# Kernel tuning notes

Measured on AMD Instinct MI355X. Metric: run time of the kernel, lower is better.

The kernel has to match this reference:

```python
import jax, jax.numpy as jnp
import numpy as np

M, K, N = 8192, 4096, 4096
ALPHA, BETA = 0.002, 0.0005


def setup_inputs() -> dict:
    key = jax.random.key(0)
    kx, kw, kb = jax.random.split(key, 3)
    # int8-range quantized activations and weights (stored as int32 for portability)
    x = jax.random.randint(kx, (M, K), -127, 127, dtype=jnp.int32)
    weight = jax.random.randint(kw, (N, K), -127, 127, dtype=jnp.int32)  # (out, in)
    bias = jax.random.randint(kb, (1, N), -(2**20), 2**20, dtype=jnp.int32)
    alpha = jnp.float32(ALPHA)
    beta = jnp.float32(BETA)
    return {"x": x, "weight": weight, "bias": bias, "alpha": alpha, "beta": beta}


def reference(x, weight, bias, alpha, beta):
    # int8 GEMM with int32 accumulation: acc[m, n] = sum_k x[m, k] * W[n, k]
    acc = jnp.matmul(x, weight.T, preferred_element_type=jnp.int32)  # [M, N] int32
    # CUTLASS-style epilogue: D = round(alpha * acc + beta * bias) -> int32
    y = alpha * acc.astype(jnp.float32) + beta * bias.astype(jnp.float32)
    return jnp.round(y).astype(jnp.int32)
```

## Files before the change

### kernel.cpp

```cpp
#include <hip/hip_runtime.h>
#include <hip/hip_bf16.h>
#include <stdint.h>

#define M_DIM 8192
#define N_DIM 4096
#define K_DIM 4096

#define BM 256
#define BN 256
#define BK 64
#define NT (K_DIM / BK)
#define DEPTH 4

typedef int v4i __attribute__((ext_vector_type(4)));

#define AS1C(p) ((const __attribute__((address_space(1))) void*)(p))
#define AS3(p)  ((__attribute__((address_space(3))) void*)(p))

__device__ __forceinline__ int pack4(int a, int b, int c, int d) {
  return (a & 0xff) | ((b & 0xff) << 8) | ((c & 0xff) << 16) | (d << 24);
}

__global__ void pack_both_kernel(const int* __restrict__ x, const int* __restrict__ w,
                                 char* __restrict__ A8, char* __restrict__ B8,
                                 int nA, int nTot) {
  int idx = blockIdx.x * blockDim.x + threadIdx.x;
  int stride = gridDim.x * blockDim.x;
  for (int i = idx; i < nTot; i += stride) {
    const int4* pin;
    int4* pout;
    if (i < nA) {
      pin  = (const int4*)x + 4 * (size_t)i;
      pout = (int4*)A8 + i;
    } else {
      int j = i - nA;
      pin  = (const int4*)w + 4 * (size_t)j;
      pout = (int4*)B8 + j;
    }
    int4 v0 = pin[0];
    int4 v1 = pin[1];
    int4 v2 = pin[2];
    int4 v3 = pin[3];
    int4 o;
    o.x = pack4(v0.x, v0.y, v0.z, v0.w);
    o.y = pack4(v1.x, v1.y, v1.z, v1.w);
    o.z = pack4(v2.x, v2.y, v2.z, v2.w);
    o.w = pack4(v3.x, v3.y, v3.z, v3.w);
    *pout = o;
  }
}

__global__ __launch_bounds__(512, 2) void gemm_i8_kernel(
    const char* __restrict__ A8, const char* __restrict__ B8,
    const int* __restrict__ bias, const float* __restrict__ alpha_p,
    const float* __restrict__ beta_p, int* __restrict__ out) {
  __shared__ alignas(16) char lds[DEPTH][BM * BK + BN * BK];

  const int tid  = threadIdx.x;
  const int lane = tid & 63;
  const int wave = tid >> 6;

  const int orig = blockIdx.x;
  const int swz  = (orig & 7) * (512 / 8) + (orig >> 3);
  const int bm   = (swz >> 4) * BM;
  const int bn   = (swz & 15) * BN;

  int aoff[2], boff[2], ldsoff[2];
#pragma unroll
  for (int i = 0; i < 2; ++i) {
    int linear = i * 8192 + tid * 16;
    int row = linear >> 6;
    int p   = (linear >> 4) & 3;
    int g   = p ^ ((row >> 1) & 3);
    ldsoff[i] = i * 8192 + wave * 1024;
    aoff[i] = (bm + row) * K_DIM + g * 16;
    boff[i] = (bn + row) * K_DIM + g * 16;
  }

#define STAGE_A(t)                                                                  \
  do {                                                                              \
    const char* ab_ = A8 + (t) * BK;                                                \
    char* base_ = &lds[(t) & (DEPTH - 1)][0];                                       \
    _Pragma("unroll") for (int i_ = 0; i_ < 2; ++i_)                                \
      __builtin_amdgcn_global_load_lds(AS1C(ab_ + aoff[i_]),                        \
                                       AS3(base_ + ldsoff[i_]), 16, 0, 0);          \
  } while (0)

#define STAGE_B(t)                                                                  \
  do {                                                                              \
    const char* bb_ = B8 + (t) * BK;                                                \
    char* base_ = &lds[(t) & (DEPTH - 1)][0];                                       \
    _Pragma("unroll") for (int i_ = 0; i_ < 2; ++i_)                                \
      __builtin_amdgcn_global_load_lds(AS1C(bb_ + boff[i_]),                        \
                                       AS3(base_ + 16384 + ldsoff[i_]), 16, 0, 0);  \
  } while (0)

  v4i acc[8][4];
#pragma unroll
  for (int i = 0; i < 8; ++i)
#pragma unroll
    for (int j = 0; j < 4; ++j) acc[i][j] = (v4i){0, 0, 0, 0};

  const int wr = wave >> 2;
  const int wc = wave & 3;
  const int frow = lane & 15;
  const int fchunk = lane >> 4;
  const int swzoff = ((fchunk ^ ((frow >> 1) & 3)) << 4);

  v4i bf0[4], aflo0[4], bf1[4], aflo1[4], afhi[4];

#define READ0(S, t)                                                                 \
  do {                                                                              \
    const char* base_ = &lds[(t) & (DEPTH - 1)][0];                                 \
    _Pragma("unroll") for (int nj = 0; nj < 4; ++nj)                                \
      bf##S[nj] = *(const v4i*)(base_ + 16384 + (wc * 64 + nj * 16 + frow) * 64 +   \
                                swzoff);                                            \
    _Pragma("unroll") for (int mi = 0; mi < 4; ++mi)                                \
      aflo##S[mi] = *(const v4i*)(base_ + (wr * 128 + mi * 16 + frow) * 64 +        \
                                  swzoff);                                          \
  } while (0)

#define READ1(t)                                                                    \
  do {                                                                              \
    const char* base_ = &lds[(t) & (DEPTH - 1)][0];                                 \
    _Pragma("unroll") for (int mi = 0; mi < 4; ++mi)                                \
      afhi[mi] = *(const v4i*)(base_ + (wr * 128 + (mi + 4) * 16 + frow) * 64 +     \
                               swzoff);                                             \
  } while (0)

#define MFMA_LO(S)                                                                  \
  do {                                                                              \
    __builtin_amdgcn_s_setprio(1);                                                  \
    _Pragma("unroll") for (int mi = 0; mi < 4; ++mi)                                \
      _Pragma("unroll") for (int nj = 0; nj < 4; ++nj)                              \
        acc[mi][nj] = __builtin_amdgcn_mfma_i32_16x16x64_i8(aflo##S[mi], bf##S[nj], \
                                                            acc[mi][nj], 0, 0, 0); \
    __builtin_amdgcn_s_setprio(0);                                                  \
  } while (0)

#define MFMA_HI(S)                                                                  \
  do {                                                                              \
    __builtin_amdgcn_s_setprio(1);                                                  \
    _Pragma("unroll") for (int mi = 0; mi < 4; ++mi)                                \
      _Pragma("unroll") for (int nj = 0; nj < 4; ++nj)                              \
        acc[mi + 4][nj] = __builtin_amdgcn_mfma_i32_16x16x64_i8(afhi[mi], bf##S[nj],\
                                                                acc[mi + 4][nj],   \
                                                                0, 0, 0);          \
    __builtin_amdgcn_s_setprio(0);                                                  \
  } while (0)

#define TILE(t, C, N, STG, EV)                                                      \
  do {                                                                              \
    if (STG) STAGE_A((t) + 3);                                                      \
    READ1(t);                                                                       \
    MFMA_LO(C);                                                                     \
    if (STG) STAGE_B((t) + 3);                                                      \
    if ((t) + 1 < NT) READ0(N, (t) + 1);                                            \
    MFMA_HI(C);                                                                     \
    if ((EV) == 4) asm volatile("s_waitcnt vmcnt(4)" ::: "memory");                 \
    if ((EV) == 0) asm volatile("s_waitcnt vmcnt(0)" ::: "memory");                 \
    if ((EV) >= 0) __builtin_amdgcn_s_barrier();                                    \
  } while (0)

  STAGE_A(0); STAGE_B(0);
  STAGE_A(1); STAGE_B(1);
  STAGE_A(2); STAGE_B(2);
  asm volatile("s_waitcnt vmcnt(4)" ::: "memory");
  __builtin_amdgcn_s_barrier();
  READ0(0, 0);

  for (int t = 0; t < NT - 4; t += 2) {
    TILE(t, 0, 1, true, 4);
    TILE(t + 1, 1, 0, true, 4);
  }
  TILE(NT - 4, 0, 1, true, 4);
  TILE(NT - 3, 1, 0, false, 0);
  TILE(NT - 2, 0, 1, false, -1);
  TILE(NT - 1, 1, 0, false, -1);

  const float alpha = *alpha_p;
  const float beta  = *beta_p;
  const int col0 = bn + wc * 64 + frow;
  float bb4[4];
#pragma unroll
  for (int nj = 0; nj < 4; ++nj) bb4[nj] = beta * (float)bias[col0 + nj * 16];

  const int rbase = bm + wr * 128 + (lane >> 4) * 4;
#pragma unroll
  for (int mi = 0; mi < 8; ++mi) {
#pragma unroll
    for (int r = 0; r < 4; ++r) {
      size_t rowoff = (size_t)(rbase + mi * 16 + r) * N_DIM;
#pragma unroll
      for (int nj = 0; nj < 4; ++nj) {
        out[rowoff + col0 + nj * 16] =
            (int)rintf(fmaf(alpha, (float)acc[mi][nj][r], bb4[nj]));
      }
    }
  }
#undef STAGE_A
#undef STAGE_B
#undef READ0
#undef READ1
#undef MFMA_LO
#undef MFMA_HI
#undef TILE
}

__global__ void naive_kernel(const int* __restrict__ x, const int* __restrict__ w,
                             const int* __restrict__ bias,
                             const float* __restrict__ alpha_p,
                             const float* __restrict__ beta_p,
                             int* __restrict__ out) {
  size_t idx = (size_t)blockIdx.x * 256 + threadIdx.x;
  int m = (int)(idx / N_DIM);
  int n = (int)(idx % N_DIM);
  const int4* xr = (const int4*)(x + (size_t)m * K_DIM);
  const int4* wr = (const int4*)(w + (size_t)n * K_DIM);
  int acc = 0;
  for (int k = 0; k < K_DIM / 4; ++k) {
    int4 a = xr[k];
    int4 b = wr[k];
    acc += a.x * b.x + a.y * b.y + a.z * b.z + a.w * b.w;
  }
  out[idx] = (int)rintf(fmaf(*alpha_p, (float)acc, (*beta_p) * (float)bias[n]));
}

extern "C" void kernel_launch(void* const* d_in, const int* in_sizes, int n_in,
                              void* d_out, int out_size, void* d_ws, size_t ws_size,
                              hipStream_t stream) {
  const int*   x     = (const int*)d_in[0];
  const int*   w     = (const int*)d_in[1];
  const int*   bias  = (const int*)d_in[2];
  const float* alpha = (const float*)d_in[3];
  const float* beta  = (const float*)d_in[4];
  int* out = (int*)d_out;

  const size_t a8_bytes = (size_t)M_DIM * K_DIM;
  const size_t b8_bytes = (size_t)N_DIM * K_DIM;

  if (ws_size >= a8_bytes + b8_bytes) {
    char* A8 = (char*)d_ws;
    char* B8 = A8 + a8_bytes;
    const int nA = (int)(a8_bytes / 16);
    const int nTot = (int)((a8_bytes + b8_bytes) / 16);
    pack_both_kernel<<<2048, 256, 0, stream>>>(x, w, A8, B8, nA, nTot);
    const int nblk = (M_DIM / BM) * (N_DIM / BN);
    gemm_i8_kernel<<<nblk, 512, 0, stream>>>(A8, B8, bias, alpha, beta, out);
  } else {
    naive_kernel<<<(M_DIM * (size_t)N_DIM) / 256, 256, 0, stream>>>(x, w, bias, alpha, beta, out);
  }
}
```

Before: 182.1 us.

## Use 4 waves per block with 128x128 per-wave tiles instead of 8 waves

```diff
diff --git a/kernel.cpp b/kernel.cpp
--- a/kernel.cpp
+++ b/kernel.cpp
@@ -50,7 +50,7 @@
   }
 }
 
-__global__ __launch_bounds__(512, 2) void gemm_i8_kernel(
+__global__ __launch_bounds__(256, 1) void gemm_i8_kernel(
     const char* __restrict__ A8, const char* __restrict__ B8,
     const int* __restrict__ bias, const float* __restrict__ alpha_p,
     const float* __restrict__ beta_p, int* __restrict__ out) {
@@ -65,14 +65,15 @@
   const int bm   = (swz >> 4) * BM;
   const int bn   = (swz & 15) * BN;
 
-  int aoff[2], boff[2], ldsoff[2];
-#pragma unroll
-  for (int i = 0; i < 2; ++i) {
-    int linear = i * 8192 + tid * 16;
+  int aoff[4], boff[4], ldsoffA[4], ldsoffB[4];
+#pragma unroll
+  for (int i = 0; i < 4; ++i) {
+    int linear = i * 4096 + tid * 16;
     int row = linear >> 6;
     int p   = (linear >> 4) & 3;
     int g   = p ^ ((row >> 1) & 3);
-    ldsoff[i] = i * 8192 + wave * 1024;
+    ldsoffA[i] = i * 4096 + wave * 1024;
+    ldsoffB[i] = 16384 + i * 4096 + wave * 1024;
     aoff[i] = (bm + row) * K_DIM + g * 16;
     boff[i] = (bn + row) * K_DIM + g * 16;
   }
@@ -81,83 +82,78 @@
   do {                                                                              \
     const char* ab_ = A8 + (t) * BK;                                                \
     char* base_ = &lds[(t) & (DEPTH - 1)][0];                                       \
-    _Pragma("unroll") for (int i_ = 0; i_ < 2; ++i_)                                \
+    _Pragma("unroll") for (int i_ = 0; i_ < 4; ++i_)                                \
       __builtin_amdgcn_global_load_lds(AS1C(ab_ + aoff[i_]),                        \
-                                       AS3(base_ + ldsoff[i_]), 16, 0, 0);          \
+                                       AS3(base_ + ldsoffA[i_]), 16, 0, 0);         \
   } while (0)
 
 #define STAGE_B(t)                                                                  \
   do {                                                                              \
     const char* bb_ = B8 + (t) * BK;                                                \
     char* base_ = &lds[(t) & (DEPTH - 1)][0];                                       \
-    _Pragma("unroll") for (int i_ = 0; i_ < 2; ++i_)                                \
+    _Pragma("unroll") for (int i_ = 0; i_ < 4; ++i_)                                \
       __builtin_amdgcn_global_load_lds(AS1C(bb_ + boff[i_]),                        \
-                                       AS3(base_ + 16384 + ldsoff[i_]), 16, 0, 0);  \
-  } while (0)
-
-  v4i acc[8][4];
+                                       AS3(base_ + ldsoffB[i_]), 16, 0, 0);         \
+  } while (0)
+
+  v4i acc[8][8];
 #pragma unroll
   for (int i = 0; i < 8; ++i)
 #pragma unroll
-    for (int j = 0; j < 4; ++j) acc[i][j] = (v4i){0, 0, 0, 0};
-
-  const int wr = wave >> 2;
-  const int wc = wave & 3;
+    for (int j = 0; j < 8; ++j) acc[i][j] = (v4i){0, 0, 0, 0};
+
+  const int wr = wave >> 1;
+  const int wc = wave & 1;
   const int frow = lane & 15;
   const int fchunk = lane >> 4;
   const int swzoff = ((fchunk ^ ((frow >> 1) & 3)) << 4);
 
-  v4i bf0[4], aflo0[4], bf1[4], aflo1[4], afhi[4];
-
-#define READ0(S, t)                                                                 \
+  v4i af0[8], bf0[8], af1[8], bf1[8];
+
+#define READ_A(S, t)                                                                \
   do {                                                                              \
     const char* base_ = &lds[(t) & (DEPTH - 1)][0];                                 \
-    _Pragma("unroll") for (int nj = 0; nj < 4; ++nj)                                \
-      bf##S[nj] = *(const v4i*)(base_ + 16384 + (wc * 64 + nj * 16 + frow) * 64 +   \
-                                swzoff);                                            \
-    _Pragma("unroll") for (int mi = 0; mi < 4; ++mi)                                \
-      aflo##S[mi] = *(const v4i*)(base_ + (wr * 128 + mi * 16 + frow) * 64 +        \
-                                  swzoff);                                          \
-  } while (0)
-
-#define READ1(t)                                                                    \
+    _Pragma("unroll") for (int mi = 0; mi < 8; ++mi)                                \
+      af##S[mi] = *(const v4i*)(base_ + (wr * 128 + mi * 16 + frow) * 64 + swzoff); \
+  } while (0)
+
+#define READ_B(S, t)                                                                \
   do {                                                                              \
     const char* base_ = &lds[(t) & (DEPTH - 1)][0];                                 \
-    _Pragma("unroll") for (int mi = 0; mi < 4; ++mi)                                \
-      afhi[mi] = *(const v4i*)(base_ + (wr * 128 + (mi + 4) * 16 + frow) * 64 +     \
-                               swzoff);                                             \
-  } while (0)
-
-#define MFMA_LO(S)                                                                  \
+    _Pragma("unroll") for (int nj = 0; nj < 8; ++nj)                                \
+      bf##S[nj] = *(const v4i*)(base_ + 16384 +                                     \
+                                (wc * 128 + nj * 16 + frow) * 64 + swzoff);         \
+  } while (0)
+
+#define MFMA_H1(S)                                                                  \
   do {                                                                              \
     __builtin_amdgcn_s_setprio(1);                                                  \
     _Pragma("unroll") for (int mi = 0; mi < 4; ++mi)                                \
-      _Pragma("unroll") for (int nj = 0; nj < 4; ++nj)                              \
-        acc[mi][nj] = __builtin_amdgcn_mfma_i32_16x16x64_i8(aflo##S[mi], bf##S[nj], \
+      _Pragma("unroll") for (int nj = 0; nj < 8; ++nj)                              \
+        acc[mi][nj] = __builtin_amdgcn_mfma_i32_16x16x64_i8(af##S[mi], bf##S[nj],   \
                                                             acc[mi][nj], 0, 0, 0); \
     __builtin_amdgcn_s_setprio(0);                                                  \
   } while (0)
 
-#define MFMA_HI(S)                                                                  \
+#define MFMA_H2(S)                                                                  \
   do {                                                                              \
     __builtin_amdgcn_s_setprio(1);                                                  \
-    _Pragma("unroll") for (int mi = 0; mi < 4; ++mi)                                \
-      _Pragma("unroll") for (int nj = 0; nj < 4; ++nj)                              \
-        acc[mi + 4][nj] = __builtin_amdgcn_mfma_i32_16x16x64_i8(afhi[mi], bf##S[nj],\
-                                                                acc[mi + 4][nj],   \
-                                                                0, 0, 0);          \
+    _Pragma("unroll") for (int mi = 4; mi < 8; ++mi)                                \
+      _Pragma("unroll") for (int nj = 0; nj < 8; ++nj)                              \
+        acc[mi][nj] = __builtin_amdgcn_mfma_i32_16x16x64_i8(af##S[mi], bf##S[nj],   \
+                                                            acc[mi][nj], 0, 0, 0); \
     __builtin_amdgcn_s_setprio(0);                                                  \
   } while (0)
 
 #define TILE(t, C, N, STG, EV)                                                      \
   do {                                                                              \
     if (STG) STAGE_A((t) + 3);                                                      \
-    READ1(t);                                                                       \
-    MFMA_LO(C);                                                                     \
+    if ((t) + 1 < NT) READ_A(N, (t) + 1);                                           \
+    MFMA_H1(C);                                                                     \
     if (STG) STAGE_B((t) + 3);                                                      \
-    if ((t) + 1 < NT) READ0(N, (t) + 1);                                            \
-    MFMA_HI(C);                                                                     \
-    if ((EV) == 4) asm volatile("s_waitcnt vmcnt(4)" ::: "memory");                 \
+    if ((t) + 1 < NT) READ_B(N, (t) + 1);                                           \
+    MFMA_H2(C);                                                                     \
+    if ((EV) == 8) asm volatile("s_waitcnt vmcnt(8)" ::: "memory");                 \
     if ((EV) == 0) asm volatile("s_waitcnt vmcnt(0)" ::: "memory");                 \
     if ((EV) >= 0) __builtin_amdgcn_s_barrier();                                    \
   } while (0)
@@ -165,25 +161,25 @@
   STAGE_A(0); STAGE_B(0);
   STAGE_A(1); STAGE_B(1);
   STAGE_A(2); STAGE_B(2);
-  asm volatile("s_waitcnt vmcnt(4)" ::: "memory");
+  asm volatile("s_waitcnt vmcnt(8)" ::: "memory");
   __builtin_amdgcn_s_barrier();
-  READ0(0, 0);
+  READ_A(0, 0); READ_B(0, 0);
 
   for (int t = 0; t < NT - 4; t += 2) {
-    TILE(t, 0, 1, true, 4);
-    TILE(t + 1, 1, 0, true, 4);
-  }
-  TILE(NT - 4, 0, 1, true, 4);
+    TILE(t, 0, 1, true, 8);
+    TILE(t + 1, 1, 0, true, 8);
+  }
+  TILE(NT - 4, 0, 1, true, 8);
   TILE(NT - 3, 1, 0, false, 0);
   TILE(NT - 2, 0, 1, false, -1);
   TILE(NT - 1, 1, 0, false, -1);
 
   const float alpha = *alpha_p;
   const float beta  = *beta_p;
-  const int col0 = bn + wc * 64 + frow;
-  float bb4[4];
-#pragma unroll
-  for (int nj = 0; nj < 4; ++nj) bb4[nj] = beta * (float)bias[col0 + nj * 16];
+  const int col0 = bn + wc * 128 + frow;
+  float bb8[8];
+#pragma unroll
+  for (int nj = 0; nj < 8; ++nj) bb8[nj] = beta * (float)bias[col0 + nj * 16];
 
   const int rbase = bm + wr * 128 + (lane >> 4) * 4;
 #pragma unroll
@@ -192,18 +188,18 @@
     for (int r = 0; r < 4; ++r) {
       size_t rowoff = (size_t)(rbase + mi * 16 + r) * N_DIM;
 #pragma unroll
-      for (int nj = 0; nj < 4; ++nj) {
+      for (int nj = 0; nj < 8; ++nj) {
         out[rowoff + col0 + nj * 16] =
-            (int)rintf(fmaf(alpha, (float)acc[mi][nj][r], bb4[nj]));
+            (int)rintf(fmaf(alpha, (float)acc[mi][nj][r], bb8[nj]));
       }
     }
   }
 #undef STAGE_A
 #undef STAGE_B
-#undef READ0
-#undef READ1
-#undef MFMA_LO
-#undef MFMA_HI
+#undef READ_A
+#undef READ_B
+#undef MFMA_H1
+#undef MFMA_H2
 #undef TILE
 }
 
@@ -246,7 +242,7 @@
     const int nTot = (int)((a8_bytes + b8_bytes) / 16);
     pack_both_kernel<<<2048, 256, 0, stream>>>(x, w, A8, B8, nA, nTot);
     const int nblk = (M_DIM / BM) * (N_DIM / BN);
-    gemm_i8_kernel<<<nblk, 512, 0, stream>>>(A8, B8, bias, alpha, beta, out);
+    gemm_i8_kernel<<<nblk, 256, 0, stream>>>(A8, B8, bias, alpha, beta, out);
   } else {
     naive_kernel<<<(M_DIM * (size_t)N_DIM) / 256, 256, 0, stream>>>(x, w, bias, alpha, beta, out);
   }
```

After: 187.1 us. 1.03x slower.

## Load B fragments directly from global into registers, bypassing LDS

Applied to the files above, without the earlier changes.

```diff
diff --git a/kernel.cpp b/kernel.cpp
--- a/kernel.cpp
+++ b/kernel.cpp
@@ -54,7 +54,7 @@
     const char* __restrict__ A8, const char* __restrict__ B8,
     const int* __restrict__ bias, const float* __restrict__ alpha_p,
     const float* __restrict__ beta_p, int* __restrict__ out) {
-  __shared__ alignas(16) char lds[DEPTH][BM * BK + BN * BK];
+  __shared__ alignas(16) char lds[DEPTH][BM * BK];
 
   const int tid  = threadIdx.x;
   const int lane = tid & 63;
@@ -65,7 +65,7 @@
   const int bm   = (swz >> 4) * BM;
   const int bn   = (swz & 15) * BN;
 
-  int aoff[2], boff[2], ldsoff[2];
+  int aoff[2], ldsoff[2];
 #pragma unroll
   for (int i = 0; i < 2; ++i) {
     int linear = i * 8192 + tid * 16;
@@ -74,25 +74,15 @@
     int g   = p ^ ((row >> 1) & 3);
     ldsoff[i] = i * 8192 + wave * 1024;
     aoff[i] = (bm + row) * K_DIM + g * 16;
-    boff[i] = (bn + row) * K_DIM + g * 16;
   }
 
 #define STAGE_A(t)                                                                  \
   do {                                                                              \
-    const char* ab_ = A8 + (t) * BK;                                                \
+    const char* ab_ = A8 + (size_t)(t) * BK;                                        \
     char* base_ = &lds[(t) & (DEPTH - 1)][0];                                       \
     _Pragma("unroll") for (int i_ = 0; i_ < 2; ++i_)                                \
       __builtin_amdgcn_global_load_lds(AS1C(ab_ + aoff[i_]),                        \
                                        AS3(base_ + ldsoff[i_]), 16, 0, 0);          \
-  } while (0)
-
-#define STAGE_B(t)                                                                  \
-  do {                                                                              \
-    const char* bb_ = B8 + (t) * BK;                                                \
-    char* base_ = &lds[(t) & (DEPTH - 1)][0];                                       \
-    _Pragma("unroll") for (int i_ = 0; i_ < 2; ++i_)                                \
-      __builtin_amdgcn_global_load_lds(AS1C(bb_ + boff[i_]),                        \
-                                       AS3(base_ + 16384 + ldsoff[i_]), 16, 0, 0);  \
   } while (0)
 
   v4i acc[8][4];
@@ -107,20 +97,25 @@
   const int fchunk = lane >> 4;
   const int swzoff = ((fchunk ^ ((frow >> 1) & 3)) << 4);
 
+  const char* Bgp = B8 + (size_t)((bn + wc * 64 + frow) * K_DIM + fchunk * 16);
+
   v4i bf0[4], aflo0[4], bf1[4], aflo1[4], afhi[4];
 
-#define READ0(S, t)                                                                 \
+#define BLOAD(S, t)                                                                 \
+  do {                                                                              \
+    _Pragma("unroll") for (int nj = 0; nj < 4; ++nj)                                \
+      bf##S[nj] = *(const v4i*)(Bgp + nj * (16 * K_DIM) + (t) * 64);                \
+  } while (0)
+
+#define READ_ALO(S, t)                                                              \
   do {                                                                              \
     const char* base_ = &lds[(t) & (DEPTH - 1)][0];                                 \
-    _Pragma("unroll") for (int nj = 0; nj < 4; ++nj)                                \
-      bf##S[nj] = *(const v4i*)(base_ + 16384 + (wc * 64 + nj * 16 + frow) * 64 +   \
-                                swzoff);                                            \
     _Pragma("unroll") for (int mi = 0; mi < 4; ++mi)                                \
       aflo##S[mi] = *(const v4i*)(base_ + (wr * 128 + mi * 16 + frow) * 64 +        \
                                   swzoff);                                          \
   } while (0)
 
-#define READ1(t)                                                                    \
+#define READ_HI(t)                                                                  \
   do {                                                                              \
     const char* base_ = &lds[(t) & (DEPTH - 1)][0];                                 \
     _Pragma("unroll") for (int mi = 0; mi < 4; ++mi)                                \
@@ -149,34 +144,35 @@
     __builtin_amdgcn_s_setprio(0);                                                  \
   } while (0)
 
-#define TILE(t, C, N, STG, EV)                                                      \
-  do {                                                                              \
-    if (STG) STAGE_A((t) + 3);                                                      \
-    READ1(t);                                                                       \
+#define TILE(t, C, N, DOBL, DOSTG, EV)                                              \
+  do {                                                                              \
+    if (DOBL) BLOAD(N, (t) + 1);                                                    \
+    if (DOSTG) STAGE_A((t) + 3);                                                    \
+    READ_HI(t);                                                                     \
     MFMA_LO(C);                                                                     \
-    if (STG) STAGE_B((t) + 3);                                                      \
-    if ((t) + 1 < NT) READ0(N, (t) + 1);                                            \
+    if ((t) + 1 < NT) READ_ALO(N, (t) + 1);                                         \
     MFMA_HI(C);                                                                     \
-    if ((EV) == 4) asm volatile("s_waitcnt vmcnt(4)" ::: "memory");                 \
+    if ((EV) == 2) asm volatile("s_waitcnt vmcnt(2)" ::: "memory");                 \
     if ((EV) == 0) asm volatile("s_waitcnt vmcnt(0)" ::: "memory");                 \
     if ((EV) >= 0) __builtin_amdgcn_s_barrier();                                    \
   } while (0)
 
-  STAGE_A(0); STAGE_B(0);
-  STAGE_A(1); STAGE_B(1);
-  STAGE_A(2); STAGE_B(2);
+  STAGE_A(0);
+  STAGE_A(1);
+  STAGE_A(2);
+  BLOAD(0, 0);
   asm volatile("s_waitcnt vmcnt(4)" ::: "memory");
   __builtin_amdgcn_s_barrier();
-  READ0(0, 0);
+  READ_ALO(0, 0);
 
   for (int t = 0; t < NT - 4; t += 2) {
-    TILE(t, 0, 1, true, 4);
-    TILE(t + 1, 1, 0, true, 4);
-  }
-  TILE(NT - 4, 0, 1, true, 4);
-  TILE(NT - 3, 1, 0, false, 0);
-  TILE(NT - 2, 0, 1, false, -1);
-  TILE(NT - 1, 1, 0, false, -1);
+    TILE(t, 0, 1, true, true, 2);
+    TILE(t + 1, 1, 0, true, true, 2);
+  }
+  TILE(NT - 4, 0, 1, true, true, 2);
+  TILE(NT - 3, 1, 0, true, false, 0);
+  TILE(NT - 2, 0, 1, true, false, 0);
+  TILE(NT - 1, 1, 0, false, false, -1);
 
   const float alpha = *alpha_p;
   const float beta  = *beta_p;
@@ -199,9 +195,9 @@
     }
   }
 #undef STAGE_A
-#undef STAGE_B
-#undef READ0
-#undef READ1
+#undef BLOAD
+#undef READ_ALO
+#undef READ_HI
 #undef MFMA_LO
 #undef MFMA_HI
 #undef TILE
```

After: 244.1 us. 1.34x slower.
